# Optimization experiments

Measured on AMD Instinct MI355X. Metric: run time of the kernel, lower is better.

Reference implementation:

```python
import jax, jax.numpy as jnp
import numpy as np


def _chord_mask(n):
    # Chord-protocol sparsity: mask[i, i] = 1 and mask[i, (i + 2**j) % n] = 1
    m = np.zeros((n, n), dtype=np.float32)
    idx = np.arange(n)
    m[idx, idx] = 1.0
    for j in range(int(np.log2(n))):
        m[idx, (idx + 2 ** j) % n] = 1.0
    return jnp.asarray(m)


def setup_inputs() -> dict:
    key = jax.random.key(0)
    ks = jax.random.split(key, 8)
    B, n_vec, n_dim = 16, 1024, 64
    n_hidden, n_W, n_class = 32, 10, 10
    data = jax.random.normal(ks[0], (B, n_vec, n_dim), dtype=jnp.float32)
    s1 = 1.0 / np.sqrt(n_dim)
    s2 = 1.0 / np.sqrt(n_hidden)
    s3 = 1.0 / np.sqrt(n_vec * n_dim)
    fW1 = jax.random.uniform(ks[1], (n_W, n_dim, n_hidden), jnp.float32, -s1, s1)
    fb1 = jax.random.uniform(ks[2], (n_W, n_hidden), jnp.float32, -s1, s1)
    fW2 = jax.random.uniform(ks[3], (n_W, n_hidden, n_vec), jnp.float32, -s2, s2)
    fb2 = jax.random.uniform(ks[4], (n_W, n_vec), jnp.float32, -s2, s2)
    final_W = jax.random.uniform(ks[5], (n_vec * n_dim, n_class), jnp.float32, -s3, s3)
    final_b = jax.random.uniform(ks[6], (n_class,), jnp.float32, -s3, s3)
    return {"data": data, "fW1": fW1, "fb1": fb1, "fW2": fW2, "fb2": fb2,
            "final_W": final_W, "final_b": final_b}


def reference(data, fW1, fb1, fW2, fb2, final_W, final_b):
    B, n_vec, n_dim = data.shape
    n_W = fW1.shape[0]
    mask = _chord_mask(n_vec)  # [n_vec, n_vec], static constant
    V = data
    residual = V
    # fs[::-1] -> iterate layers in reverse order
    for i in range(n_W - 1, -1, -1):
        h = jax.nn.gelu(jnp.einsum('bnd,dh->bnh', data, fW1[i]) + fb1[i],
                        approximate=False)
        W = jnp.einsum('bnh,hm->bnm', h, fW2[i]) + fb2[i]  # [B, n_vec, n_vec]
        W = W * mask
        V = jnp.einsum('bnm,bmd->bnd', W, V) + residual
        residual = V  # residual_every=True
    flat = V.reshape(B, n_vec * n_dim)
    return flat @ final_W + final_b
```

## Files before the change

### kernel.cpp

```cpp
#include <hip/hip_runtime.h>

#define BATCH 16
#define NVEC 1024
#define NDIM 64
#define NHID 32
#define NW   10
#define NCLS 10
#define NOFF 11
#define WPAD 12

__global__ __launch_bounds__(256) void k_transpose(
    const float* __restrict__ fW2, float* __restrict__ W2T)
{
    __shared__ float tile[NHID][65];
    const int i = blockIdx.y;
    const int m0 = blockIdx.x * 64;
    const int t = threadIdx.x;
    const int tL = t & 63, wv = t >> 6;

    const float* src = fW2 + (size_t)i * NHID * NVEC;
    #pragma unroll
    for (int jj = 0; jj < 8; ++jj) {
        int j = wv * 8 + jj;
        tile[j][tL] = src[(size_t)j * NVEC + m0 + tL];
    }
    __syncthreads();

    float* dst = W2T + (size_t)i * NVEC * NHID;
    const int j = t & 31, mrow = t >> 5;
    #pragma unroll
    for (int g = 0; g < 8; ++g) {
        int m = g * 8 + mrow;
        dst[(size_t)(m0 + m) * NHID + j] = tile[j][m];
    }
}

__global__ __launch_bounds__(256) void k_weights(
    const float* __restrict__ data,
    const float* __restrict__ fW1,
    const float* __restrict__ fb1,
    const float* __restrict__ W2T,
    const float* __restrict__ fb2,
    float* __restrict__ Wsp)
{
    const int i = blockIdx.y;
    const int nbase = blockIdx.x * 8;
    const int t = threadIdx.x;
    const int b  = t & 15;
    const int jq = (t >> 4) & 3;
    const int nl = t >> 6;
    const int j0 = jq * 8;

    __shared__ float sW1[NDIM * NHID];
    __shared__ float sb1[NHID];
    {
        const float4* w1v = (const float4*)(fW1 + (size_t)i * NDIM * NHID);
        float4* s4 = (float4*)sW1;
        for (int k = t; k < NDIM * NHID / 4; k += 256) s4[k] = w1v[k];
        if (t < NHID) sb1[t] = fb1[i * NHID + t];
    }
    __syncthreads();

    float h[2][8];
    #pragma unroll
    for (int r = 0; r < 2; ++r)
        #pragma unroll
        for (int jj = 0; jj < 8; ++jj) h[r][jj] = sb1[j0 + jj];

    const int n0 = nbase + nl * 2;
    const float4* arow0 = (const float4*)(data + ((size_t)(b * NVEC) + n0) * NDIM);
    const float4* arow1 = (const float4*)(data + ((size_t)(b * NVEC) + n0 + 1) * NDIM);

    #pragma unroll 4
    for (int g = 0; g < 16; ++g) {
        float4 a0 = arow0[g];
        float4 a1 = arow1[g];
        float as0[4] = {a0.x, a0.y, a0.z, a0.w};
        float as1[4] = {a1.x, a1.y, a1.z, a1.w};
        #pragma unroll
        for (int dk = 0; dk < 4; ++dk) {
            const float4* wp = (const float4*)(&sW1[(g * 4 + dk) * NHID + j0]);
            float4 w0 = wp[0], w1 = wp[1];
            const float wf[8] = {w0.x, w0.y, w0.z, w0.w, w1.x, w1.y, w1.z, w1.w};
            #pragma unroll
            for (int jj = 0; jj < 8; ++jj) {
                h[0][jj] += as0[dk] * wf[jj];
                h[1][jj] += as1[dk] * wf[jj];
            }
        }
    }

    #pragma unroll
    for (int r = 0; r < 2; ++r)
        #pragma unroll
        for (int jj = 0; jj < 8; ++jj) {
            float x = h[r][jj];
            h[r][jj] = 0.5f * x * (1.0f + erff(x * 0.70710678118654752f));
        }

    const float* w2t = W2T + (size_t)i * NVEC * NHID;
    const float* b2  = fb2 + (size_t)i * NVEC;
    #pragma unroll
    for (int r = 0; r < 2; ++r) {
        const int n = n0 + r;
        float* wout = Wsp + ((size_t)(i * BATCH + b) * NVEC + n) * WPAD;
        #pragma unroll
        for (int o = 0; o < NOFF; ++o) {
            int off = (o == 0) ? 0 : (1 << (o - 1));
            int m = (n + off) & (NVEC - 1);
            const float4* gp = (const float4*)(w2t + (size_t)m * NHID + j0);
            float4 g0 = gp[0], g1 = gp[1];
            float w = h[r][0] * g0.x + h[r][1] * g0.y + h[r][2] * g0.z + h[r][3] * g0.w
                    + h[r][4] * g1.x + h[r][5] * g1.y + h[r][6] * g1.z + h[r][7] * g1.w;
            w += __shfl_xor(w, 16, 64);
            w += __shfl_xor(w, 32, 64);
            if (jq == (o & 3)) wout[o] = w + b2[m];
        }
    }
}

__global__ __launch_bounds__(1024) void k_chain(
    const float* __restrict__ data,
    const float* __restrict__ Wsp,
    const float* __restrict__ Wf,
    float* __restrict__ part)
{
    const int chunk = blockIdx.x;
    const int b     = blockIdx.y;
    const int d0    = chunk * 4;
    const int n     = threadIdx.x;

    __shared__ float4 bufA[NVEC];
    __shared__ float4 bufB[NVEC];

    bufA[n] = *(const float4*)(data + ((size_t)(b * NVEC) + n) * NDIM + d0);

    const float4* wp = (const float4*)(Wsp + ((size_t)((NW - 1) * BATCH + b) * NVEC + n) * WPAD);
    float4 wa = wp[0], wb4 = wp[1], wc = wp[2];
    __syncthreads();

    float4* cur = bufA;
    float4* nxt = bufB;

    for (int l = 0; l < NW; ++l) {
        float4 na, nb, nc;
        if (l < NW - 1) {
            const float4* wpn = (const float4*)(
                Wsp + ((size_t)((NW - 2 - l) * BATCH + b) * NVEC + n) * WPAD);
            na = wpn[0]; nb = wpn[1]; nc = wpn[2];
        }
        const float wgt[12] = {wa.x, wa.y, wa.z, wa.w,
                               wb4.x, wb4.y, wb4.z, wb4.w,
                               wc.x, wc.y, wc.z, wc.w};
        float4 v0 = cur[n];
        float4 acc;
        acc.x = v0.x + wgt[0] * v0.x;
        acc.y = v0.y + wgt[0] * v0.y;
        acc.z = v0.z + wgt[0] * v0.z;
        acc.w = v0.w + wgt[0] * v0.w;
        #pragma unroll
        for (int o = 1; o < NOFF; ++o) {
            int off = 1 << (o - 1);
            float4 vv = cur[(n + off) & (NVEC - 1)];
            acc.x += wgt[o] * vv.x; acc.y += wgt[o] * vv.y;
            acc.z += wgt[o] * vv.z; acc.w += wgt[o] * vv.w;
        }
        nxt[n] = acc;
        __syncthreads();
        float4* tmp = cur; cur = nxt; nxt = tmp;
        if (l < NW - 1) { wa = na; wb4 = nb; wc = nc; }
    }

    float p[NCLS];
    #pragma unroll
    for (int c = 0; c < NCLS; ++c) p[c] = 0.0f;
    {
        float4 vv = cur[n];
        float vs[4] = {vv.x, vv.y, vv.z, vv.w};
        const float4* wfv = (const float4*)(Wf + ((size_t)(n * NDIM + d0)) * NCLS);
        float wf[40];
        #pragma unroll
        for (int k = 0; k < 10; ++k) {
            float4 u = wfv[k];
            wf[k * 4 + 0] = u.x; wf[k * 4 + 1] = u.y;
            wf[k * 4 + 2] = u.z; wf[k * 4 + 3] = u.w;
        }
        #pragma unroll
        for (int d = 0; d < 4; ++d)
            #pragma unroll
            for (int cls = 0; cls < NCLS; ++cls)
                p[cls] += vs[d] * wf[d * NCLS + cls];
    }

    const int lane = n & 63, wv = n >> 6;
    float* sred = (float*)nxt;
    #pragma unroll
    for (int cls = 0; cls < NCLS; ++cls) {
        float v = p[cls];
        #pragma unroll
        for (int s = 32; s > 0; s >>= 1) v += __shfl_down(v, s, 64);
        if (lane == 0) sred[wv * NCLS + cls] = v;
    }
    __syncthreads();
    if (n < NCLS) {
        float s = 0.0f;
        #pragma unroll
        for (int w = 0; w < 16; ++w) s += sred[w * NCLS + n];
        part[(size_t)(b * 16 + chunk) * NCLS + n] = s;
    }
}

__global__ __launch_bounds__(256) void k_finish(
    const float* __restrict__ part, const float* __restrict__ bias,
    float* __restrict__ out)
{
    int t = threadIdx.x;
    if (t < BATCH * NCLS) {
        int b = t / NCLS, cls = t % NCLS;
        float s = bias[cls];
        #pragma unroll
        for (int ch = 0; ch < 16; ++ch) s += part[(size_t)(b * 16 + ch) * NCLS + cls];
        out[t] = s;
    }
}

extern "C" void kernel_launch(void* const* d_in, const int* in_sizes, int n_in,
                              void* d_out, int out_size, void* d_ws, size_t ws_size,
                              hipStream_t stream) {
    const float* data = (const float*)d_in[0];
    const float* fW1  = (const float*)d_in[1];
    const float* fb1  = (const float*)d_in[2];
    const float* fW2  = (const float*)d_in[3];
    const float* fb2  = (const float*)d_in[4];
    const float* fWf  = (const float*)d_in[5];
    const float* fbf  = (const float*)d_in[6];
    float* out = (float*)d_out;

    float* ws   = (float*)d_ws;
    float* Wsp  = ws;
    float* W2T  = Wsp + (size_t)NW * BATCH * NVEC * WPAD;
    float* part = W2T + (size_t)NW * NVEC * NHID;

    k_transpose<<<dim3(NVEC / 64, NW), 256, 0, stream>>>(fW2, W2T);
    k_weights<<<dim3(NVEC / 8, NW), 256, 0, stream>>>(
        data, fW1, fb1, W2T, fb2, Wsp);
    k_chain<<<dim3(NDIM / 4, BATCH), 1024, 0, stream>>>(data, Wsp, fWf, part);
    k_finish<<<dim3(1), 256, 0, stream>>>(part, fbf, out);
}
```

Measured before the change: 129.1 us.

## Drop transpose and finish kernels; stage fW2 columns in shared memory

Removes the separate fW2 transpose kernel. Each k_weights block now gathers the 64 fW2 columns and fb2 entries its 8 rows touch through the chord offsets into padded shared memory, and stages its outputs in shared memory so they go out as coalesced float4 stores. The final reduction kernel is folded into k_chain with a per-batch atomic counter, where the last chunk block sums the partials and adds the bias. k_chain also keeps each thread's own vector in a register instead of rereading it from shared memory. Together this cuts two kernel launches and some global traffic, at the cost of strided gathers from fW2 and extra shared memory per block.

```diff
diff --git a/kernel.cpp b/kernel.cpp
--- a/kernel.cpp
+++ b/kernel.cpp
@@ -8,40 +8,17 @@
 #define NCLS 10
 #define NOFF 11
 #define WPAD 12
-
-__global__ __launch_bounds__(256) void k_transpose(
-    const float* __restrict__ fW2, float* __restrict__ W2T)
-{
-    __shared__ float tile[NHID][65];
-    const int i = blockIdx.y;
-    const int m0 = blockIdx.x * 64;
-    const int t = threadIdx.x;
-    const int tL = t & 63, wv = t >> 6;
-
-    const float* src = fW2 + (size_t)i * NHID * NVEC;
-    #pragma unroll
-    for (int jj = 0; jj < 8; ++jj) {
-        int j = wv * 8 + jj;
-        tile[j][tL] = src[(size_t)j * NVEC + m0 + tL];
-    }
-    __syncthreads();
-
-    float* dst = W2T + (size_t)i * NVEC * NHID;
-    const int j = t & 31, mrow = t >> 5;
-    #pragma unroll
-    for (int g = 0; g < 8; ++g) {
-        int m = g * 8 + mrow;
-        dst[(size_t)(m0 + m) * NHID + j] = tile[j][m];
-    }
-}
+#define NCHUNK (NDIM / 4)
+#define W2PAD 36
 
 __global__ __launch_bounds__(256) void k_weights(
     const float* __restrict__ data,
     const float* __restrict__ fW1,
     const float* __restrict__ fb1,
-    const float* __restrict__ W2T,
+    const float* __restrict__ fW2,
     const float* __restrict__ fb2,
-    float* __restrict__ Wsp)
+    float* __restrict__ Wsp,
+    int* __restrict__ cnt)
 {
     const int i = blockIdx.y;
     const int nbase = blockIdx.x * 8;
@@ -51,13 +28,38 @@
     const int nl = t >> 6;
     const int j0 = jq * 8;
 
-    __shared__ float sW1[NDIM * NHID];
+    __shared__ __align__(16) float sW1[NDIM * NHID];
     __shared__ float sb1[NHID];
+    __shared__ __align__(16) float sW2r[64 * W2PAD];
+    __shared__ float sb2[64];
+    __shared__ __align__(16) float rws[128 * WPAD];
+
+    if (blockIdx.x == 0 && i == 0 && t < BATCH) cnt[t] = 0;
+
     {
         const float4* w1v = (const float4*)(fW1 + (size_t)i * NDIM * NHID);
         float4* s4 = (float4*)sW1;
+        #pragma unroll
         for (int k = t; k < NDIM * NHID / 4; k += 256) s4[k] = w1v[k];
         if (t < NHID) sb1[t] = fb1[i * NHID + t];
+
+        const int j  = t >> 3;
+        const int s0 = t & 7;
+        const float* w2 = fW2 + ((size_t)i * NHID + j) * NVEC;
+        #pragma unroll
+        for (int c = 0; c < 8; ++c) {
+            int s = s0 + c * 8;
+            int k = (s < 24) ? s : ((32 << ((s - 24) >> 3)) + ((s - 24) & 7));
+            int m = (nbase + k) & (NVEC - 1);
+            sW2r[s * W2PAD + j] = w2[m];
+        }
+        if (t < 64) {
+            int s = t;
+            int k = (s < 24) ? s : ((32 << ((s - 24) >> 3)) + ((s - 24) & 7));
+            int m = (nbase + k) & (NVEC - 1);
+            sb2[s] = fb2[(size_t)i * NVEC + m];
+        }
+        for (int k = t; k < 128; k += 256) rws[k * WPAD + (WPAD - 1)] = 0.0f;
     }
     __syncthreads();
 
@@ -98,23 +100,39 @@
             h[r][jj] = 0.5f * x * (1.0f + erff(x * 0.70710678118654752f));
         }
 
-    const float* w2t = W2T + (size_t)i * NVEC * NHID;
-    const float* b2  = fb2 + (size_t)i * NVEC;
+    const int rbase = nl * 2;
     #pragma unroll
     for (int r = 0; r < 2; ++r) {
-        const int n = n0 + r;
-        float* wout = Wsp + ((size_t)(i * BATCH + b) * NVEC + n) * WPAD;
         #pragma unroll
         for (int o = 0; o < NOFF; ++o) {
-            int off = (o == 0) ? 0 : (1 << (o - 1));
-            int m = (n + off) & (NVEC - 1);
-            const float4* gp = (const float4*)(w2t + (size_t)m * NHID + j0);
+            int slot;
+            if (o == 0) slot = rbase + r;
+            else {
+                int off = 1 << (o - 1);
+                slot = (off <= 16) ? (rbase + r + off)
+                                   : (24 + 8 * (o - 6) + rbase + r);
+            }
+            const float4* gp = (const float4*)(sW2r + slot * W2PAD + j0);
             float4 g0 = gp[0], g1 = gp[1];
             float w = h[r][0] * g0.x + h[r][1] * g0.y + h[r][2] * g0.z + h[r][3] * g0.w
                     + h[r][4] * g1.x + h[r][5] * g1.y + h[r][6] * g1.z + h[r][7] * g1.w;
             w += __shfl_xor(w, 16, 64);
             w += __shfl_xor(w, 32, 64);
-            if (jq == (o & 3)) wout[o] = w + b2[m];
+            if (jq == (o & 3))
+                rws[(b * 8 + rbase + r) * WPAD + o] = w + sb2[slot];
+        }
+    }
+    __syncthreads();
+
+    {
+        const float4* rv = (const float4*)rws;
+        #pragma unroll
+        for (int k = t; k < 128 * 3; k += 256) {
+            int row = k / 3, comp = k - row * 3;
+            int bb = row >> 3, nloc = row & 7;
+            float4* dst = (float4*)(Wsp +
+                ((size_t)(i * BATCH + bb) * NVEC + nbase + nloc) * WPAD + comp * 4);
+            *dst = rv[k];
         }
     }
 }
@@ -123,7 +141,10 @@
     const float* __restrict__ data,
     const float* __restrict__ Wsp,
     const float* __restrict__ Wf,
-    float* __restrict__ part)
+    const float* __restrict__ bias,
+    float* __restrict__ part,
+    int* __restrict__ cnt,
+    float* __restrict__ out)
 {
     const int chunk = blockIdx.x;
     const int b     = blockIdx.y;
@@ -132,8 +153,10 @@
 
     __shared__ float4 bufA[NVEC];
     __shared__ float4 bufB[NVEC];
-
-    bufA[n] = *(const float4*)(data + ((size_t)(b * NVEC) + n) * NDIM + d0);
+    __shared__ int sdone;
+
+    float4 vown = *(const float4*)(data + ((size_t)(b * NVEC) + n) * NDIM + d0);
+    bufA[n] = vown;
 
     const float4* wp = (const float4*)(Wsp + ((size_t)((NW - 1) * BATCH + b) * NVEC + n) * WPAD);
     float4 wa = wp[0], wb4 = wp[1], wc = wp[2];
@@ -152,7 +175,7 @@
         const float wgt[12] = {wa.x, wa.y, wa.z, wa.w,
                                wb4.x, wb4.y, wb4.z, wb4.w,
                                wc.x, wc.y, wc.z, wc.w};
-        float4 v0 = cur[n];
+        float4 v0 = vown;
         float4 acc;
         acc.x = v0.x + wgt[0] * v0.x;
         acc.y = v0.y + wgt[0] * v0.y;
@@ -166,6 +189,7 @@
             acc.z += wgt[o] * vv.z; acc.w += wgt[o] * vv.w;
         }
         nxt[n] = acc;
+        vown = acc;
         __syncthreads();
         float4* tmp = cur; cur = nxt; nxt = tmp;
         if (l < NW - 1) { wa = na; wb4 = nb; wc = nc; }
@@ -175,8 +199,7 @@
     #pragma unroll
     for (int c = 0; c < NCLS; ++c) p[c] = 0.0f;
     {
-        float4 vv = cur[n];
-        float vs[4] = {vv.x, vv.y, vv.z, vv.w};
+        float vs[4] = {vown.x, vown.y, vown.z, vown.w};
         const float4* wfv = (const float4*)(Wf + ((size_t)(n * NDIM + d0)) * NCLS);
         float wf[40];
         #pragma unroll
@@ -206,21 +229,22 @@
         float s = 0.0f;
         #pragma unroll
         for (int w = 0; w < 16; ++w) s += sred[w * NCLS + n];
-        part[(size_t)(b * 16 + chunk) * NCLS + n] = s;
-    }
-}
-
-__global__ __launch_bounds__(256) void k_finish(
-    const float* __restrict__ part, const float* __restrict__ bias,
-    float* __restrict__ out)
-{
-    int t = threadIdx.x;
-    if (t < BATCH * NCLS) {
-        int b = t / NCLS, cls = t % NCLS;
-        float s = bias[cls];
-        #pragma unroll
-        for (int ch = 0; ch < 16; ++ch) s += part[(size_t)(b * 16 + ch) * NCLS + cls];
-        out[t] = s;
+        part[(size_t)(b * NCHUNK + chunk) * NCLS + n] = s;
+    }
+
+    __threadfence();
+    __syncthreads();
+    if (n == 0) {
+        int old = atomicAdd(cnt + b, 1);
+        sdone = (old == NCHUNK - 1);
+    }
+    __syncthreads();
+    if (sdone && n < NCLS) {
+        float s = bias[n];
+        #pragma unroll
+        for (int ch = 0; ch < NCHUNK; ++ch)
+            s += part[(size_t)(b * NCHUNK + ch) * NCLS + n];
+        out[b * NCLS + n] = s;
     }
 }
 
@@ -238,12 +262,11 @@
 
     float* ws   = (float*)d_ws;
     float* Wsp  = ws;
-    float* W2T  = Wsp + (size_t)NW * BATCH * NVEC * WPAD;
-    float* part = W2T + (size_t)NW * NVEC * NHID;
-
-    k_transpose<<<dim3(NVEC / 64, NW), 256, 0, stream>>>(fW2, W2T);
+    float* part = Wsp + (size_t)NW * BATCH * NVEC * WPAD;
+    int*   cnt  = (int*)(part + (size_t)BATCH * NCHUNK * NCLS);
+
     k_weights<<<dim3(NVEC / 8, NW), 256, 0, stream>>>(
-        data, fW1, fb1, W2T, fb2, Wsp);
-    k_chain<<<dim3(NDIM / 4, BATCH), 1024, 0, stream>>>(data, Wsp, fWf, part);
-    k_finish<<<dim3(1), 256, 0, stream>>>(part, fbf, out);
+        data, fW1, fb1, fW2, fb2, Wsp, cnt);
+    k_chain<<<dim3(NCHUNK, BATCH), 1024, 0, stream>>>(
+        data, Wsp, fWf, fbf, part, cnt, out);
 }
```

Measured after the change: 176.2 us. 36.5% more time.
